# Performance work log

Measured on AMD Instinct MI355X. Metric: run time of the kernel, lower is better.

Reference implementation:

```python
import jax, jax.numpy as jnp
import numpy as np

# ---- static config (mirrors init_kwargs) ----
CVAE = 16
VOCAB = 1 << CVAE
V_PATCH_NUMS = (1, 2, 4, 8, 16, 32)
SN = len(V_PATCH_NUMS)
NUM_LATENT_TOKENS = 1024
H = W = 32
BETA = 0.25
ENTROPY_WEIGHT = 0.1
INV_TEMP = 100.0          # temperature 0.01 as in entropy_loss default
EPS = 1e-5
W_SAMPLE_MIN = 1.0
W_BATCH_MAX = 1.0
QUANT_RESI = 0.5
N_PHI = 4                 # share_quant_resi=4 -> PhiPartiallyShared


def _phi_index():
    ticks = (np.linspace(1/3/N_PHI, 1 - 1/3/N_PHI, N_PHI) if N_PHI == 4
             else np.linspace(1/2/N_PHI, 1 - 1/2/N_PHI, N_PHI))
    return [int(np.argmin(np.abs(ticks - si / (SN - 1)))) for si in range(SN)]

PHI_IDX = _phi_index()


def _cubic(t, a=-0.75):  # torch bicubic kernel (a=-0.75)
    t = abs(t)
    if t <= 1.0:
        return (a + 2) * t**3 - (a + 3) * t**2 + 1.0
    if t < 2.0:
        return a * t**3 - 5 * a * t**2 + 8 * a * t - 4 * a
    return 0.0


def _up_matrix(n_in, n_out):
    # exact torch F.interpolate(mode='bicubic', align_corners=False) as a linear map
    M = np.zeros((n_out, n_in), np.float32)
    for i in range(n_out):
        x = (i + 0.5) * n_in / n_out - 0.5
        x0 = int(np.floor(x))
        for k in range(-1, 3):
            j = min(max(x0 + k, 0), n_in - 1)
            M[i, j] += _cubic(x - (x0 + k))
    return M

UP_MATS = {pn: jnp.asarray(_up_matrix(pn, H)) for pn in V_PATCH_NUMS if pn != H}


def area_down(x, pn):  # F.interpolate(mode='area') for divisor sizes == block mean
    B, C, Hh, Ww = x.shape
    return x.reshape(B, C, pn, Hh // pn, pn, Ww // pn).mean((3, 5))


def bicubic_up(x, pn):
    M = UP_MATS[pn]
    return jnp.einsum('hp,bcpq,wq->bchw', M, x, M)


def phi_apply(h, w, b):  # Phi: h*(1-r) + conv3x3(h)*r, r=0.5
    conv = jax.lax.conv_general_dilated(
        h, w, (1, 1), 'SAME', dimension_numbers=('NCHW', 'OIHW', 'NCHW'))
    conv = conv + b[None, :, None, None]
    return h * (1.0 - QUANT_RESI) + conv * QUANT_RESI


def lfq_forward(f_BChw, phi_w, phi_b):
    f = f_BChw.astype(jnp.float32)
    B, C, Hh, Ww = f.shape
    f_ng = jax.lax.stop_gradient(f)
    f_rest = f_ng
    f_hat = jnp.zeros_like(f)
    bitpos = jnp.arange(CVAE, dtype=jnp.int32)
    vq_loss = 0.0
    commit_loss = 0.0
    ent_loss = 0.0
    vocab_hit = jnp.zeros((SN, VOCAB), jnp.float32)
    for si, pn in enumerate(V_PATCH_NUMS):
        cv = 1.0  # scaler[si] = scale**si, scale=1
        last_direct = (si == SN - 1) and (pn == int(np.sqrt(NUM_LATENT_TOKENS)))
        rest = f_rest if last_direct else area_down(f_rest, pn)
        bits = (rest > 0)                                   # sign quantization
        # bits->index (channel-last order matches permute(0,2,3,1))
        idx = jnp.sum(bits.transpose(0, 2, 3, 1).astype(jnp.int32) << bitpos, axis=-1)  # (B,pn,pn)
        hit = jax.ops.segment_sum(jnp.ones((B * pn * pn,), jnp.float32),
                                  idx.reshape(-1), num_segments=VOCAB)
        vocab_hit = vocab_hit.at[si].add(hit)
        # index -> {-cv,+cv} codes: (B,pn,pn,C) -> (B,C,pn,pn)
        code_bits = ((idx[..., None] >> bitpos) & 1).astype(jnp.float32)
        h_small = ((code_bits * 2.0 - 1.0) * cv).transpose(0, 3, 1, 2)
        h = h_small if si == SN - 1 else bicubic_up(h_small, pn)
        h = phi_apply(h, phi_w[PHI_IDX[si]], phi_b[PHI_IDX[si]])
        # residual before this step, shape b (h w) 1 d
        x = (f - jax.lax.stop_gradient(f_hat)).transpose(0, 2, 3, 1).reshape(B, Hh * Ww, 1, C)
        f_hat = f_hat + h      # eval: mask all ones, ratio=1
        f_rest = f_rest - h
        # soft entropy loss (analytical per-sample, per-bit binary probabilities)
        p = jax.nn.sigmoid(-4.0 * x / cv * INV_TEMP)        # (B,HW,1,C)
        prob = jnp.stack([p, 1.0 - p], axis=-1)             # (B,HW,1,C,2)
        sample_ent = -(prob * jnp.log(prob + EPS)).sum(-1)  # per-bit entropy
        per_sample_entropy = sample_ent.sum(-1).mean()
        avg_prob = prob.mean((0, 1, 2))                     # (C,2)
        codebook_entropy = -(avg_prob * jnp.log(avg_prob + EPS)).sum()
        ent_loss = ent_loss + (W_SAMPLE_MIN * per_sample_entropy
                               - W_BATCH_MAX * codebook_entropy)
        vq_loss = vq_loss + jnp.mean((f_hat - f_ng) ** 2)
        commit_loss = commit_loss + BETA * jnp.mean((jax.lax.stop_gradient(f_hat) - f) ** 2)
    vq_loss = vq_loss / SN
    commit_loss = commit_loss / SN
    ent_loss = ent_loss * (ENTROPY_WEIGHT / SN)
    f_hat_out = jax.lax.stop_gradient(f_hat - f_ng) + f     # straight-through estimator
    total = vq_loss + commit_loss + ent_loss
    return f_hat_out, total, vocab_hit


def setup_inputs() -> dict:
    key = jax.random.key(0)
    k1, k2 = jax.random.split(key)
    f = jax.random.normal(k1, (256, 16, 32, 32), dtype=jnp.float32)
    phi_w = jax.random.normal(k2, (N_PHI, CVAE, CVAE, 3, 3), dtype=jnp.float32) * 0.05
    phi_b = jnp.zeros((N_PHI, CVAE), dtype=jnp.float32)
    return {"f_BChw": f, "phi_w": phi_w, "phi_b": phi_b}


def reference(f_BChw, phi_w, phi_b):
    return lfq_forward(f_BChw, phi_w, phi_b)
```

## Files before the change

kernel.cpp:

```cpp
#include <hip/hip_runtime.h>

#define VOCAB 65536
#define NELEM 4194304
#define BHW   262144

__device__ __forceinline__ double cubic_d(double t) {
  const double a = -0.75;
  t = fabs(t);
  if (t <= 1.0) return ((a + 2.0) * t - (a + 3.0)) * t * t + 1.0;
  if (t < 2.0)  return a * (((t - 5.0) * t + 8.0) * t - 4.0);
  return 0.0;
}

__device__ __forceinline__ int idx32_slot(int x, int y) { return (x << 5) | ((y ^ x) & 31); }

template<int PN>
__device__ __forceinline__ void process_scale(
    int si, int phi_idx, bool load_w,
    const float* __restrict__ f, const float* __restrict__ phi_w,
    const float* __restrict__ phi_b, float* __restrict__ hist,
    double* __restrict__ acc, double (&fhat)[4][4],
    double* __restrict__ hupd, float* __restrict__ wlds,
    unsigned* __restrict__ idxL, float* __restrict__ wMT,
    float* __restrict__ bias16, double* __restrict__ red,
    int t, int y, int g, int x0, size_t ibase)
{
  constexpr int CELLS = PN * PN;
  constexpr int S = 32 / PN;
  const int w = t >> 6;

  idxL[t] = 0u;
  if (load_w) {
    for (int i = t; i < 2304; i += 1024) wlds[i] = phi_w[phi_idx * 2304 + i];
    if (t < 16) bias16[t] = phi_b[phi_idx * 16 + t];
  }
  if constexpr (PN != 32) {
    if (t < 32) {
      float wrow[PN];
      #pragma unroll
      for (int q = 0; q < PN; ++q) wrow[q] = 0.0f;
      double xp = ((double)t + 0.5) * (double)PN / 32.0 - 0.5;
      int q0 = (int)floor(xp);
      for (int k = 0; k < 4; ++k) {
        int j = q0 + k - 1;
        int jc = j < 0 ? 0 : (j > PN - 1 ? PN - 1 : j);
        wrow[jc] += (float)cubic_d(xp - (double)j);
      }
      #pragma unroll
      for (int q = 0; q < PN; ++q) wMT[q * 32 + t] = wrow[q];
    }
    float entf = 0.0f;
    float ps[4];
    #pragma unroll
    for (int cc = 0; cc < 4; ++cc) {
      const float4 fv = *(const float4*)(f + ibase + (size_t)(4 * g + cc) * 1024 + y * 32 + x0);
      double* hp = hupd + (4 * g + cc) * 1056 + y * 33 + x0;
      float psl = 0.0f;
      float fvk[4] = {fv.x, fv.y, fv.z, fv.w};
      #pragma unroll
      for (int k = 0; k < 4; ++k) {
        double xr = (double)fvk[k] - fhat[cc][k];
        hp[k] = xr;
        float pr = 1.0f / (1.0f + __expf(400.0f * (float)xr));
        entf -= pr * __logf(pr + 1e-5f) + (1.0f - pr) * __logf(1.0f - pr + 1e-5f);
        psl += pr;
      }
      ps[cc] = psl;
    }
    double ent_d = (double)entf;
    #pragma unroll
    for (int off = 32; off > 0; off >>= 1) {
      ent_d += __shfl_down(ent_d, off);
      ps[0] += __shfl_down(ps[0], off);
      ps[1] += __shfl_down(ps[1], off);
      ps[2] += __shfl_down(ps[2], off);
      ps[3] += __shfl_down(ps[3], off);
    }
    if ((t & 63) == 0) {
      red[w * 6 + 1] = ent_d;
      red[w * 6 + 2] = (double)ps[0];
      red[w * 6 + 3] = (double)ps[1];
      red[w * 6 + 4] = (double)ps[2];
      red[w * 6 + 5] = (double)ps[3];
    }
  }
  __syncthreads();

  if constexpr (PN == 32) {
    float entf = 0.0f;
    float ps[4];
    unsigned bb[4] = {0u, 0u, 0u, 0u};
    #pragma unroll
    for (int cc = 0; cc < 4; ++cc) {
      const float4 fv = *(const float4*)(f + ibase + (size_t)(4 * g + cc) * 1024 + y * 32 + x0);
      float psl = 0.0f;
      float fvk[4] = {fv.x, fv.y, fv.z, fv.w};
      #pragma unroll
      for (int k = 0; k < 4; ++k) {
        double xr = (double)fvk[k] - fhat[cc][k];
        if (xr > 0.0) bb[k] |= (1u << cc);
        float pr = 1.0f / (1.0f + __expf(400.0f * (float)xr));
        entf -= pr * __logf(pr + 1e-5f) + (1.0f - pr) * __logf(1.0f - pr + 1e-5f);
        psl += pr;
      }
      ps[cc] = psl;
    }
    #pragma unroll
    for (int k = 0; k < 4; ++k)
      if (bb[k]) atomicOr(&idxL[idx32_slot(x0 + k, y)], bb[k] << (4 * g));
    double ent_d = (double)entf;
    #pragma unroll
    for (int off = 32; off > 0; off >>= 1) {
      ent_d += __shfl_down(ent_d, off);
      ps[0] += __shfl_down(ps[0], off);
      ps[1] += __shfl_down(ps[1], off);
      ps[2] += __shfl_down(ps[2], off);
      ps[3] += __shfl_down(ps[3], off);
    }
    if ((t & 63) == 0) {
      red[w * 6 + 1] = ent_d;
      red[w * 6 + 2] = (double)ps[0];
      red[w * 6 + 3] = (double)ps[1];
      red[w * 6 + 4] = (double)ps[2];
      red[w * 6 + 5] = (double)ps[3];
    }
  } else if constexpr (PN == 16) {
    int cell = t & 255;
    int i0 = (cell >> 4) * 2, j0 = (cell & 15) * 2;
    unsigned bits = 0;
    #pragma unroll
    for (int k = 0; k < 4; ++k) {
      int c = (t >> 8) + 4 * k;
      const double* hp = hupd + c * 1056 + i0 * 33 + j0;
      double s = hp[0] + hp[1] + hp[33] + hp[34];
      if (s > 0.0) bits |= (1u << c);
    }
    atomicOr(&idxL[cell], bits);
  } else if constexpr (PN == 8) {
    int c = t >> 6, cell = t & 63;
    const double* hp = hupd + c * 1056 + ((cell >> 3) * 4) * 33 + (cell & 7) * 4;
    double s = 0.0;
    #pragma unroll
    for (int dy = 0; dy < 4; ++dy)
      #pragma unroll
      for (int dx = 0; dx < 4; ++dx) s += hp[dy * 33 + dx];
    if (s > 0.0) atomicOr(&idxL[cell], 1u << c);
  } else {
    constexpr int TASKS = 16 * CELLS;
    constexpr int G = 1024 / TASKS;
    int p = t / G, sub = t % G;
    int c = p / CELLS, cell = p % CELLS;
    const double* hp = hupd + c * 1056 + ((cell / PN) * S) * 33 + (cell % PN) * S;
    double s = 0.0;
    for (int e = sub; e < S * S; e += G) {
      int dy = e / S, dx = e % S;
      s += hp[dy * 33 + dx];
    }
    #pragma unroll
    for (int off = G / 2; off > 0; off >>= 1) s += __shfl_down(s, off, G);
    if (sub == 0 && s > 0.0) atomicOr(&idxL[cell], 1u << c);
  }
  __syncthreads();

  if constexpr (PN == 32) {
    atomicAdd(&hist[5 * VOCAB + idxL[t]], 1.0f);
  } else {
    if (t < CELLS) atomicAdd(&hist[(size_t)si * VOCAB + idxL[t]], 1.0f);
  }
  {
    int c2 = t >> 6, sub = (t >> 5) & 1, y2 = t & 31;
    double* hrow = hupd + c2 * 1056 + y2 * 33;
    if constexpr (PN == 32) {
      #pragma unroll
      for (int xi = 0; xi < 16; ++xi) {
        int x = 16 * sub + xi;
        hrow[x] = ((idxL[idx32_slot(x, y2)] >> c2) & 1) ? 1.0 : -1.0;
      }
    } else {
      constexpr int QC = (PN < 4) ? PN : 4;
      #pragma unroll
      for (int q0 = 0; q0 < PN; q0 += QC) {
        double tmp[QC];
        #pragma unroll
        for (int qq = 0; qq < QC; ++qq) tmp[qq] = 0.0;
        #pragma unroll
        for (int r = 0; r < PN; ++r) {
          double ww = (double)wMT[r * 32 + y2];
          #pragma unroll
          for (int qq = 0; qq < QC; ++qq) {
            double sg = ((idxL[r * PN + q0 + qq] >> c2) & 1) ? 1.0 : -1.0;
            tmp[qq] = fma(ww, sg, tmp[qq]);
          }
        }
        #pragma unroll
        for (int xi = 0; xi < 16; ++xi) {
          int x = 16 * sub + xi;
          double s2 = (q0 == 0) ? 0.0 : hrow[x];
          #pragma unroll
          for (int qq = 0; qq < QC; ++qq)
            s2 = fma((double)wMT[(q0 + qq) * 32 + x], tmp[qq], s2);
          hrow[x] = s2;
        }
      }
    }
  }
  __syncthreads();

  #pragma unroll
  for (int cc = 0; cc < 4; ++cc) {
    double bh = 0.5 * (double)bias16[4 * g + cc];
    const double* hu = hupd + (4 * g + cc) * 1056 + y * 33 + x0;
    #pragma unroll
    for (int k = 0; k < 4; ++k)
      fhat[cc][k] = fhat[cc][k] + 0.5 * hu[k] + bh;
  }

  for (int ci = 0; ci < 16; ++ci) {
    const double* hbase = hupd + ci * 1056;
    #pragma unroll
    for (int dy = 0; dy < 3; ++dy) {
      int ry = y + dy - 1;
      if (ry < 0 || ry > 31) continue;
      double prow[6];
      const double* hr = hbase + ry * 33;
      #pragma unroll
      for (int jj = 0; jj < 6; ++jj) {
        int xx = x0 - 1 + jj;
        prow[jj] = (xx < 0 || xx > 31) ? 0.0 : hr[xx];
      }
      #pragma unroll
      for (int cc = 0; cc < 4; ++cc) {
        const float* wp = wlds + (((4 * g + cc) * 16 + ci) * 9 + dy * 3);
        double w0 = 0.5 * (double)wp[0], w1 = 0.5 * (double)wp[1], w2 = 0.5 * (double)wp[2];
        #pragma unroll
        for (int k = 0; k < 4; ++k)
          fhat[cc][k] = fma(w0, prow[k], fma(w1, prow[k + 1], fma(w2, prow[k + 2], fhat[cc][k])));
      }
    }
  }

  double mse = 0.0;
  #pragma unroll
  for (int cc = 0; cc < 4; ++cc) {
    const float4 fv = *(const float4*)(f + ibase + (size_t)(4 * g + cc) * 1024 + y * 32 + x0);
    float fvk[4] = {fv.x, fv.y, fv.z, fv.w};
    #pragma unroll
    for (int k = 0; k < 4; ++k) {
      double d = fhat[cc][k] - (double)fvk[k];
      mse += d * d;
    }
  }
  #pragma unroll
  for (int off = 32; off > 0; off >>= 1) mse += __shfl_down(mse, off);
  if ((t & 63) == 0) red[w * 6 + 0] = mse;
  __syncthreads();

  if (t == 0) {
    double m = 0.0, e = 0.0;
    #pragma unroll
    for (int ww = 0; ww < 16; ++ww) { m += red[ww * 6]; e += red[ww * 6 + 1]; }
    atomicAdd(&acc[si * 18 + 0], m);
    atomicAdd(&acc[si * 18 + 1], e);
  }
  if (t < 16) {
    int gg = t >> 2, cc = t & 3;
    double p = red[(4 * gg + 0) * 6 + 2 + cc] + red[(4 * gg + 1) * 6 + 2 + cc]
             + red[(4 * gg + 2) * 6 + 2 + cc] + red[(4 * gg + 3) * 6 + 2 + cc];
    atomicAdd(&acc[si * 18 + 2 + t], p);
  }
  __syncthreads();
}

__global__ __launch_bounds__(1024) void lfq_all(
    const float* __restrict__ f, const float* __restrict__ phi_w,
    const float* __restrict__ phi_b, float* __restrict__ fhi,
    float* __restrict__ hist, double* __restrict__ acc)
{
  __shared__ double   hupd[16 * 1056];
  __shared__ float    wlds[2304];
  __shared__ unsigned idxL[1024];
  __shared__ float    wMT[512];
  __shared__ float    bias16[16];
  __shared__ double   red[96];

  const int t = threadIdx.x;
  const int y = (t >> 3) & 31, g = t >> 8;
  const int x0 = (t & 7) * 4;
  const size_t ibase = (size_t)blockIdx.x * 16384;

  double fhat[4][4];
  #pragma unroll
  for (int cc = 0; cc < 4; ++cc)
    #pragma unroll
    for (int k = 0; k < 4; ++k) fhat[cc][k] = 0.0;

  process_scale<1 >(0, 0, true,  f, phi_w, phi_b, hist, acc, fhat, hupd, wlds, idxL, wMT, bias16, red, t, y, g, x0, ibase);
  process_scale<2 >(1, 0, false, f, phi_w, phi_b, hist, acc, fhat, hupd, wlds, idxL, wMT, bias16, red, t, y, g, x0, ibase);
  process_scale<4 >(2, 1, true,  f, phi_w, phi_b, hist, acc, fhat, hupd, wlds, idxL, wMT, bias16, red, t, y, g, x0, ibase);
  process_scale<8 >(3, 2, true,  f, phi_w, phi_b, hist, acc, fhat, hupd, wlds, idxL, wMT, bias16, red, t, y, g, x0, ibase);
  process_scale<16>(4, 3, true,  f, phi_w, phi_b, hist, acc, fhat, hupd, wlds, idxL, wMT, bias16, red, t, y, g, x0, ibase);
  process_scale<32>(5, 3, false, f, phi_w, phi_b, hist, acc, fhat, hupd, wlds, idxL, wMT, bias16, red, t, y, g, x0, ibase);

  #pragma unroll
  for (int cc = 0; cc < 4; ++cc) {
    float* op = fhi + ibase + (size_t)(4 * g + cc) * 1024 + y * 32 + x0;
    #pragma unroll
    for (int k = 0; k < 4; ++k) op[k] = (float)fhat[cc][k];
  }
}

__global__ void finalize_total(const double* __restrict__ acc, float* __restrict__ total)
{
  if (threadIdx.x == 0 && blockIdx.x == 0) {
    double vq = 0.0, ent = 0.0;
    for (int si = 0; si < 6; ++si) {
      vq += acc[si * 18 + 0];
      double pse = acc[si * 18 + 1] / (double)BHW;
      double ce = 0.0;
      for (int cc = 0; cc < 16; ++cc) {
        double ap0 = acc[si * 18 + 2 + cc] / (double)BHW;
        double ap1 = 1.0 - ap0;
        ce -= ap0 * log(ap0 + 1e-5) + ap1 * log(ap1 + 1e-5);
      }
      ent += pse - ce;
    }
    *total = (float)(1.25 * vq / ((double)NELEM * 6.0) + (0.1 / 6.0) * ent);
  }
}

extern "C" void kernel_launch(void* const* d_in, const int* in_sizes, int n_in,
                              void* d_out, int out_size, void* d_ws, size_t ws_size,
                              hipStream_t stream)
{
  const float* f     = (const float*)d_in[0];
  const float* phi_w = (const float*)d_in[1];
  const float* phi_b = (const float*)d_in[2];
  float* out   = (float*)d_out;
  float* fhi   = out;
  float* total = out + NELEM;
  float* hist  = out + NELEM + 1;
  double* acc  = (double*)d_ws;

  hipMemsetAsync((void*)(out + NELEM), 0, (size_t)(1 + 6 * VOCAB) * sizeof(float), stream);
  hipMemsetAsync(d_ws, 0, 1024, stream);

  lfq_all<<<256, 1024, 0, stream>>>(f, phi_w, phi_b, fhi, hist, acc);
  finalize_total<<<1, 64, 0, stream>>>(acc, total);
}
```

Before: 370.9 us.

## Halve block size, give each thread 8 pixels, fold MSE into next scale

Blocks drop from 1024 to 512 threads, and each thread now owns 8 consecutive pixels per channel instead of 4. This gives wider register tiles for the 3x3 conv, so the row halo loads are reused across more outputs. The per-scale MSE reduction and its extra barrier are removed: each scale's MSE is taken from the residual computed at the start of the next scale, and a final MSE pass runs after the last scale. Output stores become float4. The cost is more registers per thread (fhat is now 32 doubles) and fewer waves per block, which could reduce latency hiding with only 256 blocks launched.

```diff
diff --git a/kernel.cpp b/kernel.cpp
--- a/kernel.cpp
+++ b/kernel.cpp
@@ -19,7 +19,7 @@
     int si, int phi_idx, bool load_w,
     const float* __restrict__ f, const float* __restrict__ phi_w,
     const float* __restrict__ phi_b, float* __restrict__ hist,
-    double* __restrict__ acc, double (&fhat)[4][4],
+    double* __restrict__ acc, double (&fhat)[4][8],
     double* __restrict__ hupd, float* __restrict__ wlds,
     unsigned* __restrict__ idxL, float* __restrict__ wMT,
     float* __restrict__ bias16, double* __restrict__ red,
@@ -29,133 +29,145 @@
   constexpr int S = 32 / PN;
   const int w = t >> 6;
 
-  idxL[t] = 0u;
+  idxL[t] = 0u; idxL[t + 512] = 0u;
   if (load_w) {
-    for (int i = t; i < 2304; i += 1024) wlds[i] = phi_w[phi_idx * 2304 + i];
+    for (int i = t; i < 2304; i += 512) wlds[i] = phi_w[phi_idx * 2304 + i];
     if (t < 16) bias16[t] = phi_b[phi_idx * 16 + t];
   }
   if constexpr (PN != 32) {
     if (t < 32) {
-      float wrow[PN];
-      #pragma unroll
-      for (int q = 0; q < PN; ++q) wrow[q] = 0.0f;
+      #pragma unroll
+      for (int q = 0; q < PN; ++q) wMT[q * 32 + t] = 0.0f;
       double xp = ((double)t + 0.5) * (double)PN / 32.0 - 0.5;
-      int q0 = (int)floor(xp);
+      int q0i = (int)floor(xp);
       for (int k = 0; k < 4; ++k) {
-        int j = q0 + k - 1;
+        int j = q0i + k - 1;
         int jc = j < 0 ? 0 : (j > PN - 1 ? PN - 1 : j);
-        wrow[jc] += (float)cubic_d(xp - (double)j);
-      }
-      #pragma unroll
-      for (int q = 0; q < PN; ++q) wMT[q * 32 + t] = wrow[q];
-    }
-    float entf = 0.0f;
-    float ps[4];
+        wMT[jc * 32 + t] += (float)cubic_d(xp - (double)j);
+      }
+    }
+    double mseP = 0.0;
+    float entf = 0.0f, ps0 = 0, ps1 = 0, ps2 = 0, ps3 = 0;
     #pragma unroll
     for (int cc = 0; cc < 4; ++cc) {
-      const float4 fv = *(const float4*)(f + ibase + (size_t)(4 * g + cc) * 1024 + y * 32 + x0);
+      const float* fp = f + ibase + (size_t)(4 * g + cc) * 1024 + y * 32 + x0;
+      float4 fa = *(const float4*)fp;
+      float4 fb = *(const float4*)(fp + 4);
+      float fvk[8] = {fa.x, fa.y, fa.z, fa.w, fb.x, fb.y, fb.z, fb.w};
       double* hp = hupd + (4 * g + cc) * 1056 + y * 33 + x0;
       float psl = 0.0f;
-      float fvk[4] = {fv.x, fv.y, fv.z, fv.w};
-      #pragma unroll
-      for (int k = 0; k < 4; ++k) {
+      #pragma unroll
+      for (int k = 0; k < 8; ++k) {
         double xr = (double)fvk[k] - fhat[cc][k];
         hp[k] = xr;
+        mseP += xr * xr;
         float pr = 1.0f / (1.0f + __expf(400.0f * (float)xr));
         entf -= pr * __logf(pr + 1e-5f) + (1.0f - pr) * __logf(1.0f - pr + 1e-5f);
         psl += pr;
       }
-      ps[cc] = psl;
+      if (cc == 0) ps0 = psl; else if (cc == 1) ps1 = psl; else if (cc == 2) ps2 = psl; else ps3 = psl;
     }
     double ent_d = (double)entf;
     #pragma unroll
     for (int off = 32; off > 0; off >>= 1) {
+      mseP  += __shfl_down(mseP, off);
       ent_d += __shfl_down(ent_d, off);
-      ps[0] += __shfl_down(ps[0], off);
-      ps[1] += __shfl_down(ps[1], off);
-      ps[2] += __shfl_down(ps[2], off);
-      ps[3] += __shfl_down(ps[3], off);
+      ps0 += __shfl_down(ps0, off); ps1 += __shfl_down(ps1, off);
+      ps2 += __shfl_down(ps2, off); ps3 += __shfl_down(ps3, off);
     }
     if ((t & 63) == 0) {
-      red[w * 6 + 1] = ent_d;
-      red[w * 6 + 2] = (double)ps[0];
-      red[w * 6 + 3] = (double)ps[1];
-      red[w * 6 + 4] = (double)ps[2];
-      red[w * 6 + 5] = (double)ps[3];
-    }
-  }
-  __syncthreads();
+      red[w * 8 + 0] = mseP; red[w * 8 + 1] = ent_d;
+      red[w * 8 + 2] = (double)ps0; red[w * 8 + 3] = (double)ps1;
+      red[w * 8 + 4] = (double)ps2; red[w * 8 + 5] = (double)ps3;
+    }
+  }
+  __syncthreads();
+
+  if constexpr (PN != 32) {
+    if (t == 0) {
+      double m = 0.0, e = 0.0;
+      #pragma unroll
+      for (int ww = 0; ww < 8; ++ww) { m += red[ww * 8]; e += red[ww * 8 + 1]; }
+      if (si > 0) atomicAdd(&acc[(si - 1) * 18 + 0], m);
+      atomicAdd(&acc[si * 18 + 1], e);
+    }
+    if (t < 16) {
+      int gg = t >> 2, cc = t & 3;
+      atomicAdd(&acc[si * 18 + 2 + t], red[(2 * gg) * 8 + 2 + cc] + red[(2 * gg + 1) * 8 + 2 + cc]);
+    }
+  }
 
   if constexpr (PN == 32) {
-    float entf = 0.0f;
-    float ps[4];
-    unsigned bb[4] = {0u, 0u, 0u, 0u};
+    double mseP = 0.0;
+    float entf = 0.0f, ps0 = 0, ps1 = 0, ps2 = 0, ps3 = 0;
+    unsigned bb[8] = {0, 0, 0, 0, 0, 0, 0, 0};
     #pragma unroll
     for (int cc = 0; cc < 4; ++cc) {
-      const float4 fv = *(const float4*)(f + ibase + (size_t)(4 * g + cc) * 1024 + y * 32 + x0);
+      const float* fp = f + ibase + (size_t)(4 * g + cc) * 1024 + y * 32 + x0;
+      float4 fa = *(const float4*)fp;
+      float4 fb = *(const float4*)(fp + 4);
+      float fvk[8] = {fa.x, fa.y, fa.z, fa.w, fb.x, fb.y, fb.z, fb.w};
       float psl = 0.0f;
-      float fvk[4] = {fv.x, fv.y, fv.z, fv.w};
-      #pragma unroll
-      for (int k = 0; k < 4; ++k) {
+      #pragma unroll
+      for (int k = 0; k < 8; ++k) {
         double xr = (double)fvk[k] - fhat[cc][k];
         if (xr > 0.0) bb[k] |= (1u << cc);
+        mseP += xr * xr;
         float pr = 1.0f / (1.0f + __expf(400.0f * (float)xr));
         entf -= pr * __logf(pr + 1e-5f) + (1.0f - pr) * __logf(1.0f - pr + 1e-5f);
         psl += pr;
       }
-      ps[cc] = psl;
-    }
-    #pragma unroll
-    for (int k = 0; k < 4; ++k)
+      if (cc == 0) ps0 = psl; else if (cc == 1) ps1 = psl; else if (cc == 2) ps2 = psl; else ps3 = psl;
+    }
+    #pragma unroll
+    for (int k = 0; k < 8; ++k)
       if (bb[k]) atomicOr(&idxL[idx32_slot(x0 + k, y)], bb[k] << (4 * g));
     double ent_d = (double)entf;
     #pragma unroll
     for (int off = 32; off > 0; off >>= 1) {
+      mseP  += __shfl_down(mseP, off);
       ent_d += __shfl_down(ent_d, off);
-      ps[0] += __shfl_down(ps[0], off);
-      ps[1] += __shfl_down(ps[1], off);
-      ps[2] += __shfl_down(ps[2], off);
-      ps[3] += __shfl_down(ps[3], off);
+      ps0 += __shfl_down(ps0, off); ps1 += __shfl_down(ps1, off);
+      ps2 += __shfl_down(ps2, off); ps3 += __shfl_down(ps3, off);
     }
     if ((t & 63) == 0) {
-      red[w * 6 + 1] = ent_d;
-      red[w * 6 + 2] = (double)ps[0];
-      red[w * 6 + 3] = (double)ps[1];
-      red[w * 6 + 4] = (double)ps[2];
-      red[w * 6 + 5] = (double)ps[3];
+      red[w * 8 + 0] = mseP; red[w * 8 + 1] = ent_d;
+      red[w * 8 + 2] = (double)ps0; red[w * 8 + 3] = (double)ps1;
+      red[w * 8 + 4] = (double)ps2; red[w * 8 + 5] = (double)ps3;
     }
   } else if constexpr (PN == 16) {
     int cell = t & 255;
     int i0 = (cell >> 4) * 2, j0 = (cell & 15) * 2;
     unsigned bits = 0;
     #pragma unroll
-    for (int k = 0; k < 4; ++k) {
-      int c = (t >> 8) + 4 * k;
+    for (int k = 0; k < 8; ++k) {
+      int c = (t >> 8) + 2 * k;
       const double* hp = hupd + c * 1056 + i0 * 33 + j0;
       double s = hp[0] + hp[1] + hp[33] + hp[34];
       if (s > 0.0) bits |= (1u << c);
     }
     atomicOr(&idxL[cell], bits);
   } else if constexpr (PN == 8) {
-    int c = t >> 6, cell = t & 63;
-    const double* hp = hupd + c * 1056 + ((cell >> 3) * 4) * 33 + (cell & 7) * 4;
-    double s = 0.0;
-    #pragma unroll
-    for (int dy = 0; dy < 4; ++dy)
-      #pragma unroll
-      for (int dx = 0; dx < 4; ++dx) s += hp[dy * 33 + dx];
-    if (s > 0.0) atomicOr(&idxL[cell], 1u << c);
+    #pragma unroll
+    for (int k = 0; k < 2; ++k) {
+      int task = t + 512 * k;
+      int c = task >> 6, cell = task & 63;
+      const double* hp = hupd + c * 1056 + ((cell >> 3) * 4) * 33 + (cell & 7) * 4;
+      double s = 0.0;
+      #pragma unroll
+      for (int dy = 0; dy < 4; ++dy)
+        #pragma unroll
+        for (int dx = 0; dx < 4; ++dx) s += hp[dy * 33 + dx];
+      if (s > 0.0) atomicOr(&idxL[cell], 1u << c);
+    }
   } else {
     constexpr int TASKS = 16 * CELLS;
-    constexpr int G = 1024 / TASKS;
+    constexpr int G = 512 / TASKS;
     int p = t / G, sub = t % G;
     int c = p / CELLS, cell = p % CELLS;
     const double* hp = hupd + c * 1056 + ((cell / PN) * S) * 33 + (cell % PN) * S;
     double s = 0.0;
-    for (int e = sub; e < S * S; e += G) {
-      int dy = e / S, dx = e % S;
-      s += hp[dy * 33 + dx];
-    }
+    for (int e = sub; e < S * S; e += G) s += hp[(e / S) * 33 + (e % S)];
     #pragma unroll
     for (int off = G / 2; off > 0; off >>= 1) s += __shfl_down(s, off, G);
     if (sub == 0 && s > 0.0) atomicOr(&idxL[cell], 1u << c);
@@ -163,19 +175,32 @@
   __syncthreads();
 
   if constexpr (PN == 32) {
+    if (t == 0) {
+      double m = 0.0, e = 0.0;
+      #pragma unroll
+      for (int ww = 0; ww < 8; ++ww) { m += red[ww * 8]; e += red[ww * 8 + 1]; }
+      atomicAdd(&acc[4 * 18 + 0], m);
+      atomicAdd(&acc[5 * 18 + 1], e);
+    }
+    if (t < 16) {
+      int gg = t >> 2, cc = t & 3;
+      atomicAdd(&acc[5 * 18 + 2 + t], red[(2 * gg) * 8 + 2 + cc] + red[(2 * gg + 1) * 8 + 2 + cc]);
+    }
+  }
+
+  if constexpr (PN == 32) {
     atomicAdd(&hist[5 * VOCAB + idxL[t]], 1.0f);
+    atomicAdd(&hist[5 * VOCAB + idxL[t + 512]], 1.0f);
   } else {
     if (t < CELLS) atomicAdd(&hist[(size_t)si * VOCAB + idxL[t]], 1.0f);
   }
   {
-    int c2 = t >> 6, sub = (t >> 5) & 1, y2 = t & 31;
+    int c2 = t >> 5, y2 = t & 31;
     double* hrow = hupd + c2 * 1056 + y2 * 33;
     if constexpr (PN == 32) {
       #pragma unroll
-      for (int xi = 0; xi < 16; ++xi) {
-        int x = 16 * sub + xi;
+      for (int x = 0; x < 32; ++x)
         hrow[x] = ((idxL[idx32_slot(x, y2)] >> c2) & 1) ? 1.0 : -1.0;
-      }
     } else {
       constexpr int QC = (PN < 4) ? PN : 4;
       #pragma unroll
@@ -193,8 +218,7 @@
           }
         }
         #pragma unroll
-        for (int xi = 0; xi < 16; ++xi) {
-          int x = 16 * sub + xi;
+        for (int x = 0; x < 32; ++x) {
           double s2 = (q0 == 0) ? 0.0 : hrow[x];
           #pragma unroll
           for (int qq = 0; qq < QC; ++qq)
@@ -211,20 +235,19 @@
     double bh = 0.5 * (double)bias16[4 * g + cc];
     const double* hu = hupd + (4 * g + cc) * 1056 + y * 33 + x0;
     #pragma unroll
-    for (int k = 0; k < 4; ++k)
+    for (int k = 0; k < 8; ++k)
       fhat[cc][k] = fhat[cc][k] + 0.5 * hu[k] + bh;
   }
-
   for (int ci = 0; ci < 16; ++ci) {
     const double* hbase = hupd + ci * 1056;
     #pragma unroll
     for (int dy = 0; dy < 3; ++dy) {
       int ry = y + dy - 1;
       if (ry < 0 || ry > 31) continue;
-      double prow[6];
+      double prow[10];
       const double* hr = hbase + ry * 33;
       #pragma unroll
-      for (int jj = 0; jj < 6; ++jj) {
+      for (int jj = 0; jj < 10; ++jj) {
         int xx = x0 - 1 + jj;
         prow[jj] = (xx < 0 || xx > 31) ? 0.0 : hr[xx];
       }
@@ -233,45 +256,15 @@
         const float* wp = wlds + (((4 * g + cc) * 16 + ci) * 9 + dy * 3);
         double w0 = 0.5 * (double)wp[0], w1 = 0.5 * (double)wp[1], w2 = 0.5 * (double)wp[2];
         #pragma unroll
-        for (int k = 0; k < 4; ++k)
+        for (int k = 0; k < 8; ++k)
           fhat[cc][k] = fma(w0, prow[k], fma(w1, prow[k + 1], fma(w2, prow[k + 2], fhat[cc][k])));
       }
     }
   }
-
-  double mse = 0.0;
-  #pragma unroll
-  for (int cc = 0; cc < 4; ++cc) {
-    const float4 fv = *(const float4*)(f + ibase + (size_t)(4 * g + cc) * 1024 + y * 32 + x0);
-    float fvk[4] = {fv.x, fv.y, fv.z, fv.w};
-    #pragma unroll
-    for (int k = 0; k < 4; ++k) {
-      double d = fhat[cc][k] - (double)fvk[k];
-      mse += d * d;
-    }
-  }
-  #pragma unroll
-  for (int off = 32; off > 0; off >>= 1) mse += __shfl_down(mse, off);
-  if ((t & 63) == 0) red[w * 6 + 0] = mse;
-  __syncthreads();
-
-  if (t == 0) {
-    double m = 0.0, e = 0.0;
-    #pragma unroll
-    for (int ww = 0; ww < 16; ++ww) { m += red[ww * 6]; e += red[ww * 6 + 1]; }
-    atomicAdd(&acc[si * 18 + 0], m);
-    atomicAdd(&acc[si * 18 + 1], e);
-  }
-  if (t < 16) {
-    int gg = t >> 2, cc = t & 3;
-    double p = red[(4 * gg + 0) * 6 + 2 + cc] + red[(4 * gg + 1) * 6 + 2 + cc]
-             + red[(4 * gg + 2) * 6 + 2 + cc] + red[(4 * gg + 3) * 6 + 2 + cc];
-    atomicAdd(&acc[si * 18 + 2 + t], p);
-  }
-  __syncthreads();
-}
-
-__global__ __launch_bounds__(1024) void lfq_all(
+  __syncthreads();
+}
+
+__global__ __launch_bounds__(512) void lfq_all(
     const float* __restrict__ f, const float* __restrict__ phi_w,
     const float* __restrict__ phi_b, float* __restrict__ fhi,
     float* __restrict__ hist, double* __restrict__ acc)
@@ -281,18 +274,19 @@
   __shared__ unsigned idxL[1024];
   __shared__ float    wMT[512];
   __shared__ float    bias16[16];
-  __shared__ double   red[96];
+  __shared__ double   red[64];
 
   const int t = threadIdx.x;
-  const int y = (t >> 3) & 31, g = t >> 8;
-  const int x0 = (t & 7) * 4;
+  const int y = (t >> 2) & 31, g = t >> 7;
+  const int x0 = (t & 3) * 8;
   const size_t ibase = (size_t)blockIdx.x * 16384;
-
-  double fhat[4][4];
+  const int w = t >> 6;
+
+  double fhat[4][8];
   #pragma unroll
   for (int cc = 0; cc < 4; ++cc)
     #pragma unroll
-    for (int k = 0; k < 4; ++k) fhat[cc][k] = 0.0;
+    for (int k = 0; k < 8; ++k) fhat[cc][k] = 0.0;
 
   process_scale<1 >(0, 0, true,  f, phi_w, phi_b, hist, acc, fhat, hupd, wlds, idxL, wMT, bias16, red, t, y, g, x0, ibase);
   process_scale<2 >(1, 0, false, f, phi_w, phi_b, hist, acc, fhat, hupd, wlds, idxL, wMT, bias16, red, t, y, g, x0, ibase);
@@ -301,11 +295,37 @@
   process_scale<16>(4, 3, true,  f, phi_w, phi_b, hist, acc, fhat, hupd, wlds, idxL, wMT, bias16, red, t, y, g, x0, ibase);
   process_scale<32>(5, 3, false, f, phi_w, phi_b, hist, acc, fhat, hupd, wlds, idxL, wMT, bias16, red, t, y, g, x0, ibase);
 
+  double mse = 0.0;
+  #pragma unroll
+  for (int cc = 0; cc < 4; ++cc) {
+    const float* fp = f + ibase + (size_t)(4 * g + cc) * 1024 + y * 32 + x0;
+    float4 fa = *(const float4*)fp;
+    float4 fb = *(const float4*)(fp + 4);
+    float fvk[8] = {fa.x, fa.y, fa.z, fa.w, fb.x, fb.y, fb.z, fb.w};
+    #pragma unroll
+    for (int k = 0; k < 8; ++k) {
+      double d = fhat[cc][k] - (double)fvk[k];
+      mse += d * d;
+    }
+  }
+  #pragma unroll
+  for (int off = 32; off > 0; off >>= 1) mse += __shfl_down(mse, off);
+  if ((t & 63) == 0) red[w * 8] = mse;
+  __syncthreads();
+  if (t == 0) {
+    double m = 0.0;
+    #pragma unroll
+    for (int ww = 0; ww < 8; ++ww) m += red[ww * 8];
+    atomicAdd(&acc[5 * 18 + 0], m);
+  }
+
   #pragma unroll
   for (int cc = 0; cc < 4; ++cc) {
     float* op = fhi + ibase + (size_t)(4 * g + cc) * 1024 + y * 32 + x0;
-    #pragma unroll
-    for (int k = 0; k < 4; ++k) op[k] = (float)fhat[cc][k];
+    float4 o1 = make_float4((float)fhat[cc][0], (float)fhat[cc][1], (float)fhat[cc][2], (float)fhat[cc][3]);
+    float4 o2 = make_float4((float)fhat[cc][4], (float)fhat[cc][5], (float)fhat[cc][6], (float)fhat[cc][7]);
+    *(float4*)op = o1;
+    *(float4*)(op + 4) = o2;
   }
 }
 
@@ -344,6 +364,6 @@
   hipMemsetAsync((void*)(out + NELEM), 0, (size_t)(1 + 6 * VOCAB) * sizeof(float), stream);
   hipMemsetAsync(d_ws, 0, 1024, stream);
 
-  lfq_all<<<256, 1024, 0, stream>>>(f, phi_w, phi_b, fhi, hist, acc);
+  lfq_all<<<256, 512, 0, stream>>>(f, phi_w, phi_b, fhi, hist, acc);
   finalize_total<<<1, 64, 0, stream>>>(acc, total);
 }
```

New measurement: 309.3 us. -16.6%, faster.
